# Performance work log

Hardware: AMD Instinct MI355X
Metric: run time of the kernel (lower is better)

The kernel has to match this reference:

```python
import jax, jax.numpy as jnp
import numpy as np
from jax import lax

K = 10
EPS = 1e-12

def _l2norm(v):
    # F.normalize: v / max(||v||_2, eps) along last dim
    n = jnp.sqrt(jnp.sum(v * v, axis=-1, keepdims=True))
    return v / jnp.maximum(n, EPS)

def setup_inputs() -> dict:
    key = jax.random.key(0)
    ks = jax.random.split(key, 10)
    N, F_in, H, C, E = 100000, 512, 128, 40, 1600000
    x = jax.random.normal(ks[0], (N, F_in), dtype=jnp.float32)
    edge_index = jax.random.randint(ks[1], (2, E), 0, N, dtype=jnp.int64)
    s1 = 1.0 / np.sqrt(F_in)
    W1 = jax.random.uniform(ks[2], (F_in, H), jnp.float32, -s1, s1)
    b1 = jax.random.uniform(ks[3], (H,), jnp.float32, -s1, s1)
    s2 = 1.0 / np.sqrt(H)
    proj_w = jax.random.uniform(ks[4], (H, 1), jnp.float32, -s2, s2)
    proj_b = jax.random.uniform(ks[5], (1,), jnp.float32, -s2, s2)
    hop_w = jax.random.normal(ks[6], (1, K + 1), dtype=jnp.float32) * 0.1  # glorot-ish
    W2 = jax.random.uniform(ks[7], (H, C), jnp.float32, -s2, s2)
    b2 = jax.random.uniform(ks[8], (C,), jnp.float32, -s2, s2)
    return {"x": x, "edge_index": edge_index, "W1": W1, "b1": b1,
            "proj_w": proj_w, "proj_b": proj_b, "hop_w": hop_w,
            "W2": W2, "b2": b2}

def reference(x, edge_index, W1, b1, proj_w, proj_b, hop_w, W2, b2):
    N = x.shape[0]
    # Net: dropout (eval -> identity), lin1 + selu
    h = jax.nn.selu(x @ W1 + b1)  # [N, H]

    # --- gcn_norm with added self-loops ---
    loops = jnp.arange(N, dtype=edge_index.dtype)
    row = jnp.concatenate([edge_index[0], loops])
    col = jnp.concatenate([edge_index[1], loops])
    ew = jnp.ones(row.shape[0], dtype=h.dtype)
    deg = jax.ops.segment_sum(ew, col, num_segments=N)  # [N]
    dinv = jnp.where(deg > 0, lax.rsqrt(deg), 0.0)
    norm = dinv[row] * ew * dinv[col]  # [E+N]

    # --- K hops of scatter-add propagation ---
    def hop(xc, _):
        xn = jax.ops.segment_sum(norm[:, None] * xc[row], col, num_segments=N)
        return xn, xn
    _, hops = lax.scan(hop, h, None, length=K)  # [K, N, H]
    pps = jnp.concatenate([h[None], hops], axis=0).transpose(1, 0, 2)  # [N, K+1, H]

    # attention-weighted hop pooling
    feature_pool = (pps @ proj_w + proj_b)[..., 0]      # [N, K+1]
    m = feature_pool.mean(axis=0)                        # [K+1]
    share_w = _l2norm(m + hop_w)                         # [1, K+1]
    self_w = _l2norm(feature_pool)                       # [N, K+1]
    share = jnp.einsum('k,nkh->nh', share_w[0], pps)     # [N, H]
    selfr = jnp.einsum('nk,nkh->nh', self_w, pps)        # [N, H]
    out_prop = 0.2 * share + 0.8 * selfr

    h2 = jnp.tanh(out_prop)
    logits = h2 @ W2 + b2
    return jax.nn.log_softmax(logits, axis=1)
```

## Files before the change

### kernel.cpp

```cpp
#include <hip/hip_runtime.h>

typedef unsigned int uint;
typedef unsigned short ushort;

typedef short short8 __attribute__((ext_vector_type(8)));
typedef float floatx4 __attribute__((ext_vector_type(4)));
typedef uint uintx4 __attribute__((ext_vector_type(4)));

#define FIN 512
#define HF  128
#define NC  40
#define KHOPS 10

__device__ __forceinline__ ushort f2bf(float f) {
    uint u = __float_as_uint(f);
    uint r = (u + 0x7fffu + ((u >> 16) & 1u)) >> 16;
    return (ushort)r;
}
__device__ __forceinline__ float bflo(uint v) { return __uint_as_float(v << 16); }
__device__ __forceinline__ float bfhi(uint v) { return __uint_as_float(v & 0xffff0000u); }
__device__ __forceinline__ uint packbf2(float a, float b) {
    return (uint)f2bf(a) | ((uint)f2bf(b) << 16);
}
__device__ __forceinline__ uint cvtpk(float lo, float hi) {
    uint r;
    asm("v_cvt_pk_bf16_f32 %0, %1, %2" : "=v"(r) : "v"(lo), "v"(hi));
    return r;
}
__device__ __forceinline__ float selu_f(float v) {
    const float l = 1.0507009873554805f, a = 1.6732632423543772f;
    return v > 0.f ? l * v : l * a * (expf(v) - 1.f);
}

#define GLDS16(g, l)                                                        \
    __builtin_amdgcn_global_load_lds(                                       \
        (const __attribute__((address_space(1))) void*)(g),                 \
        (__attribute__((address_space(3))) void*)(l), 16, 0, 0)

__global__ void k_w1frag(const float* __restrict__ W1, ushort* __restrict__ w1f) {
    int id = blockIdx.x * 256 + threadIdx.x;
    if (id >= 16 * 8 * 64) return;
    int l = id & 63;
    int t = (id >> 6) & 7;
    int s = id >> 9;
    int row0 = s * 32 + (l >> 4) * 8;
    int col  = t * 16 + (l & 15);
    ushort* dst = w1f + (size_t)id * 8;
#pragma unroll
    for (int i = 0; i < 8; ++i)
        dst[i] = f2bf(W1[(row0 + i) * HF + col]);
}

__global__ void k_w2frag(const float* __restrict__ W2, ushort* __restrict__ w2f) {
    int id = blockIdx.x * 256 + threadIdx.x;
    if (id >= 12 * 64) return;
    int l = id & 63;
    int tile = id >> 6;
    int kk = tile / 3, t = tile % 3;
    int row0 = kk * 32 + (l >> 4) * 8;
    int col  = t * 16 + (l & 15);
    ushort* dst = w2f + (size_t)id * 8;
#pragma unroll
    for (int i = 0; i < 8; ++i)
        dst[i] = (col < NC) ? f2bf(W2[(row0 + i) * NC + col]) : (ushort)0;
}

__global__ __launch_bounds__(256) void k_gemm(
        const float* __restrict__ x, const ushort* __restrict__ w1f,
        const float* __restrict__ b1, ushort* __restrict__ h,
        const float* __restrict__ projw, const float* __restrict__ projb,
        float* __restrict__ fp0, int N) {
    __shared__ __align__(16) float bufA[4][32 * 32];
    __shared__ __align__(16) float bufB[4][32 * 32];
    int tid = threadIdx.x;
    int lane = tid & 63, w = tid >> 6;
    int rowblk = blockIdx.x * 128 + w * 32;

    int srl = lane >> 3;
    int ssl = lane & 7;
    int srcoff = ((ssl ^ srl) << 2);
    float* bA = bufA[w];
    float* bB = bufB[w];

    floatx4 acc[2][8];
#pragma unroll
    for (int rt = 0; rt < 2; ++rt)
#pragma unroll
        for (int t = 0; t < 8; ++t) acc[rt][t] = (floatx4){0.f, 0.f, 0.f, 0.f};

    short8 bE[8], bO[8];

    auto STAGE = [&](float* lbuf, int kk) {
        int k0 = kk * 32;
#pragma unroll
        for (int i = 0; i < 4; ++i) {
            int row = rowblk + i * 8 + srl;
            const float* g = x + (size_t)min(row, N - 1) * FIN + k0 + srcoff;
            GLDS16(g, lbuf + i * 256);
        }
    };
    auto LOADB = [&](short8* bb, int kk) {
        const ushort* wp = w1f + ((size_t)(kk * 8) * 64 + lane) * 8;
#pragma unroll
        for (int t = 0; t < 8; ++t) bb[t] = *(const short8*)(wp + (size_t)t * 512);
    };

    int rl16 = lane & 15, cq = lane >> 4;
    int lo_sl = ((2 * cq) ^ (rl16 & 7)) << 4;
    int hi_sl = ((2 * cq + 1) ^ (rl16 & 7)) << 4;

    auto COMPUTE = [&](const float* lbuf, short8* bb) {
#pragma unroll
        for (int rt = 0; rt < 2; ++rt) {
            const char* rbase = (const char*)lbuf + (rt * 16 + rl16) * 128;
            float4 lo = *(const float4*)(rbase + lo_sl);
            float4 hi = *(const float4*)(rbase + hi_sl);
            uintx4 pa;
            pa.x = cvtpk(lo.x, lo.y); pa.y = cvtpk(lo.z, lo.w);
            pa.z = cvtpk(hi.x, hi.y); pa.w = cvtpk(hi.z, hi.w);
            short8 af = __builtin_bit_cast(short8, pa);
#pragma unroll
            for (int t = 0; t < 8; ++t)
                acc[rt][t] = __builtin_amdgcn_mfma_f32_16x16x32_bf16(af, bb[t], acc[rt][t], 0, 0, 0);
        }
    };

    STAGE(bA, 0);
    LOADB(bE, 0);
#pragma unroll 1
    for (int kk = 0; kk < 16; kk += 2) {
        asm volatile("s_waitcnt lgkmcnt(0)" ::: "memory");
        __builtin_amdgcn_sched_barrier(0);
        STAGE(bB, kk + 1);
        LOADB(bO, kk + 1);
        asm volatile("s_waitcnt vmcnt(12)" ::: "memory");
        __builtin_amdgcn_sched_barrier(0);
        COMPUTE(bA, bE);
        asm volatile("s_waitcnt lgkmcnt(0)" ::: "memory");
        __builtin_amdgcn_sched_barrier(0);
        if (kk + 2 < 16) {
            STAGE(bA, kk + 2);
            LOADB(bE, kk + 2);
            asm volatile("s_waitcnt vmcnt(12)" ::: "memory");
        } else {
            asm volatile("s_waitcnt vmcnt(0)" ::: "memory");
        }
        __builtin_amdgcn_sched_barrier(0);
        COMPUTE(bB, bO);
    }

    int col0 = lane & 15;
    float fpd[2][4];
#pragma unroll
    for (int rt = 0; rt < 2; ++rt)
#pragma unroll
        for (int q = 0; q < 4; ++q) fpd[rt][q] = 0.f;
#pragma unroll
    for (int t = 0; t < 8; ++t) {
        int col = t * 16 + col0;
        float bias = b1[col];
        float pw = projw[col];
#pragma unroll
        for (int rt = 0; rt < 2; ++rt) {
#pragma unroll
            for (int q = 0; q < 4; ++q) {
                int row = rowblk + rt * 16 + (lane >> 4) * 4 + q;
                float v = selu_f(acc[rt][t][q] + bias);
                if (row < N) h[(size_t)row * HF + col] = f2bf(v);
                fpd[rt][q] = fmaf(v, pw, fpd[rt][q]);
            }
        }
    }
#pragma unroll
    for (int rt = 0; rt < 2; ++rt)
#pragma unroll
        for (int q = 0; q < 4; ++q) {
            float d = fpd[rt][q];
#pragma unroll
            for (int m = 1; m < 16; m <<= 1) d += __shfl_xor(d, m);
            fpd[rt][q] = d;
        }
    if (col0 == 0) {
        float pb = projb[0];
#pragma unroll
        for (int rt = 0; rt < 2; ++rt)
#pragma unroll
            for (int q = 0; q < 4; ++q) {
                int row = rowblk + rt * 16 + (lane >> 4) * 4 + q;
                if (row < N) fp0[row] = fpd[rt][q] + pb;
            }
    }
}

__global__ void k_deg_init(int* __restrict__ deg, int N) {
    int i = blockIdx.x * 256 + threadIdx.x;
    if (i < N) deg[i] = 1;
}
__global__ void k_deg(const int* __restrict__ ei, int* __restrict__ deg, int E) {
    int e = blockIdx.x * 256 + threadIdx.x;
    if (e < E) atomicAdd(&deg[ei[E + e]], 1);
}
__global__ void k_dinv(const int* __restrict__ deg, float* __restrict__ dinv, int N) {
    int i = blockIdx.x * 256 + threadIdx.x;
    if (i < N) dinv[i] = rsqrtf((float)deg[i]);
}

__global__ void k_scan1(const int* __restrict__ deg, int* __restrict__ offs,
                        int* __restrict__ bsum, int N) {
    __shared__ int lds[256];
    int tid = threadIdx.x;
    int base = blockIdx.x * 1024;
    int c[4], s = 0;
#pragma unroll
    for (int i = 0; i < 4; ++i) {
        int g = base + tid * 4 + i;
        c[i] = (g < N) ? (deg[g] - 1) : 0;
        s += c[i];
    }
    lds[tid] = s;
    __syncthreads();
    for (int off = 1; off < 256; off <<= 1) {
        int add = (tid >= off) ? lds[tid - off] : 0;
        __syncthreads();
        lds[tid] += add;
        __syncthreads();
    }
    int run = lds[tid] - s;
#pragma unroll
    for (int i = 0; i < 4; ++i) {
        int g = base + tid * 4 + i;
        if (g < N) offs[g] = run;
        run += c[i];
    }
    if (tid == 0) bsum[blockIdx.x] = lds[255];
}
__global__ void k_scan2(int* __restrict__ bsum, int nb) {
    if (blockIdx.x == 0 && threadIdx.x == 0) {
        int run = 0;
        for (int i = 0; i < nb; ++i) { int v = bsum[i]; bsum[i] = run; run += v; }
    }
}
__global__ void k_scan3(int* __restrict__ offs, const int* __restrict__ bsum, int N, int E) {
    int g = blockIdx.x * 256 + threadIdx.x;
    if (g < N) offs[g] += bsum[g >> 10];
    else if (g == N) offs[N] = E;
}

__global__ void k_fill(const int* __restrict__ ei, const int* __restrict__ offs,
                       int* __restrict__ cursor, int2* __restrict__ edat,
                       const float* __restrict__ dinv, int E) {
    int e = blockIdx.x * 256 + threadIdx.x;
    if (e >= E) return;
    int r = ei[e], c = ei[E + e];
    int p = offs[c] + atomicAdd(&cursor[c], 1);
    edat[p] = make_int2(r, __float_as_int(dinv[r] * dinv[c]));
}

__global__ __launch_bounds__(256) void k_hop(
                      const ushort* __restrict__ xin, ushort* __restrict__ xout,
                      const int* __restrict__ offs, const int2* __restrict__ edat,
                      const float* __restrict__ dinv,
                      const float* __restrict__ projw, const float* __restrict__ projb,
                      float* __restrict__ fpk, int N) {
    int wid = (blockIdx.x * blockDim.x + threadIdx.x) >> 6;
    int lane = threadIdx.x & 63;
    if (wid >= N) return;
    const uint* xin2 = (const uint*)xin;
    float dn = dinv[wid];
    uint sv = xin2[(size_t)wid * 64 + lane];
    float wself = dn * dn;
    float acc0 = wself * bflo(sv);
    float acc1 = wself * bfhi(sv);
    int s = offs[wid], e = offs[wid + 1];
    for (int base = s; base < e; base += 64) {
        int idx = base + lane;
        int idxc = min(idx, e - 1);
        int2 ed = edat[idxc];
        int src = ed.x;
        float ew = (idx < e) ? __int_as_float(ed.y) : 0.f;
        int cnt = min(64, e - base);
        int groups = (cnt + 15) >> 4;
        for (int g = 0; g < groups; ++g) {
            int j = g * 16;
            uint xv[16];
            float wv[16];
#pragma unroll
            for (int u = 0; u < 16; ++u) {
                int sj = __builtin_amdgcn_readlane(src, j + u);
                wv[u] = __int_as_float(__builtin_amdgcn_readlane(__float_as_int(ew), j + u));
                xv[u] = xin2[(size_t)(uint)sj * 64 + lane];
            }
#pragma unroll
            for (int u = 0; u < 16; ++u) {
                acc0 = fmaf(wv[u], bflo(xv[u]), acc0);
                acc1 = fmaf(wv[u], bfhi(xv[u]), acc1);
            }
        }
    }
    ((uint*)xout)[(size_t)wid * 64 + lane] = packbf2(acc0, acc1);
    float dot = acc0 * projw[2 * lane] + acc1 * projw[2 * lane + 1];
#pragma unroll
    for (int m = 1; m < 64; m <<= 1) dot += __shfl_xor(dot, m);
    if (lane == 0) fpk[wid] = dot + projb[0];
}

__global__ void k_msum(const float* __restrict__ fp, float* __restrict__ msum, int N) {
    int k = blockIdx.y;
    int i = blockIdx.x * 256 + threadIdx.x;
    int tid = threadIdx.x;
    float v = (i < N) ? fp[(size_t)k * N + i] : 0.f;
#pragma unroll
    for (int m = 1; m < 64; m <<= 1) v += __shfl_xor(v, m);
    __shared__ float ws4[4];
    if ((tid & 63) == 0) ws4[tid >> 6] = v;
    __syncthreads();
    if (tid == 0) atomicAdd(&msum[k], ws4[0] + ws4[1] + ws4[2] + ws4[3]);
}

__global__ void k_sharew(const float* __restrict__ msum, const float* __restrict__ hopw,
                         float* __restrict__ sharew, int N) {
    int k = threadIdx.x;
    float s = (k < KHOPS + 1) ? (msum[k] / (float)N + hopw[k]) : 0.f;
    float ss = s * s;
#pragma unroll
    for (int m = 1; m < 64; m <<= 1) ss += __shfl_xor(ss, m);
    float inv = 1.f / fmaxf(sqrtf(ss), 1e-12f);
    if (k < KHOPS + 1) sharew[k] = s * inv;
}

__global__ __launch_bounds__(256) void k_out(
                     const ushort* __restrict__ hops, const float* __restrict__ fp,
                     const float* __restrict__ sharew, const ushort* __restrict__ w2f,
                     const float* __restrict__ b2, float* __restrict__ out, int N) {
    __shared__ __align__(16) char As[16 * 256];
    int tid = threadIdx.x;
    int nloc = tid >> 4;
    int fg = tid & 15;
    int node = blockIdx.x * 16 + nloc;
    bool valid = node < N;
    int nodec = valid ? node : N - 1;
    const uint* hops2 = (const uint*)hops;

    float c[KHOPS + 1];
    float ss = 0.f;
#pragma unroll
    for (int k = 0; k <= KHOPS; ++k) {
        float f = fp[(size_t)k * N + nodec];
        c[k] = f;
        ss += f * f;
    }
    float inv = 1.f / fmaxf(sqrtf(ss), 1e-12f);
#pragma unroll
    for (int k = 0; k <= KHOPS; ++k)
        c[k] = valid ? (0.2f * sharew[k] + 0.8f * c[k] * inv) : 0.f;

    const uint* base = hops2 + (size_t)nodec * 64 + fg * 4;
    size_t kstr = (size_t)N * 64;
    float a[8];
#pragma unroll
    for (int j = 0; j < 8; ++j) a[j] = 0.f;
#pragma unroll
    for (int k = 0; k <= KHOPS; ++k) {
        uint4 v = *(const uint4*)(base + (size_t)k * kstr);
        float ck = c[k];
        a[0] = fmaf(ck, bflo(v.x), a[0]);
        a[1] = fmaf(ck, bfhi(v.x), a[1]);
        a[2] = fmaf(ck, bflo(v.y), a[2]);
        a[3] = fmaf(ck, bfhi(v.y), a[3]);
        a[4] = fmaf(ck, bflo(v.z), a[4]);
        a[5] = fmaf(ck, bfhi(v.z), a[5]);
        a[6] = fmaf(ck, bflo(v.w), a[6]);
        a[7] = fmaf(ck, bfhi(v.w), a[7]);
    }
    uint4 pk;
    pk.x = packbf2(tanhf(a[0]), tanhf(a[1]));
    pk.y = packbf2(tanhf(a[2]), tanhf(a[3]));
    pk.z = packbf2(tanhf(a[4]), tanhf(a[5]));
    pk.w = packbf2(tanhf(a[6]), tanhf(a[7]));
    {
        int slotbyte = fg * 16;
        int addr = nloc * 256 + (slotbyte ^ ((nloc & 15) << 4));
        *(uint4*)(As + addr) = pk;
    }
    __syncthreads();

    int w = tid >> 6, lane = tid & 63;
    floatx4 acc = (floatx4){0.f, 0.f, 0.f, 0.f};
    if (w < 3) {
        int r = lane & 15;
#pragma unroll
        for (int kk = 0; kk < 4; ++kk) {
            int slotbyte = kk * 64 + (lane >> 4) * 16;
            int addr = r * 256 + (slotbyte ^ ((r & 15) << 4));
            short8 af = *(const short8*)(As + addr);
            const short8 bf = *(const short8*)(w2f + (size_t)((kk * 3 + w) * 64 + lane) * 8);
            acc = __builtin_amdgcn_mfma_f32_16x16x32_bf16(af, bf, acc, 0, 0, 0);
        }
    }
    __syncthreads();

    float* Ls = (float*)As;
    if (w < 3) {
        int cls = w * 16 + (lane & 15);
        float bb = (cls < NC) ? b2[cls] : 0.f;
#pragma unroll
        for (int q = 0; q < 4; ++q) {
            int row = (lane >> 4) * 4 + q;
            Ls[row * 48 + cls] = acc[q] + bb;
        }
    }
    __syncthreads();

    int r2 = tid >> 4;
    int c16 = tid & 15;
    float v0 = Ls[r2 * 48 + c16];
    float v1 = Ls[r2 * 48 + 16 + c16];
    bool has2 = c16 < 8;
    float v2 = has2 ? Ls[r2 * 48 + 32 + c16] : -INFINITY;
    float lm = fmaxf(fmaxf(v0, v1), v2);
#pragma unroll
    for (int m = 1; m < 16; m <<= 1) lm = fmaxf(lm, __shfl_xor(lm, m));
    float se = expf(v0 - lm) + expf(v1 - lm) + (has2 ? expf(v2 - lm) : 0.f);
#pragma unroll
    for (int m = 1; m < 16; m <<= 1) se += __shfl_xor(se, m);
    float lse = lm + logf(se);
    int nodeo = blockIdx.x * 16 + r2;
    if (nodeo < N) {
        out[(size_t)nodeo * NC + c16] = v0 - lse;
        out[(size_t)nodeo * NC + 16 + c16] = v1 - lse;
        if (has2) out[(size_t)nodeo * NC + 32 + c16] = v2 - lse;
    }
}

extern "C" void kernel_launch(void* const* d_in, const int* in_sizes, int n_in,
                              void* d_out, int out_size, void* d_ws, size_t ws_size,
                              hipStream_t stream) {
    const float* x     = (const float*)d_in[0];
    const int*   ei    = (const int*)d_in[1];
    const float* W1    = (const float*)d_in[2];
    const float* b1    = (const float*)d_in[3];
    const float* projw = (const float*)d_in[4];
    const float* projb = (const float*)d_in[5];
    const float* hopw  = (const float*)d_in[6];
    const float* W2    = (const float*)d_in[7];
    const float* b2    = (const float*)d_in[8];
    float* out = (float*)d_out;

    int N = in_sizes[0] / FIN;
    int E = in_sizes[1] / 2;

    char* p = (char*)d_ws;
    auto alloc = [&](size_t bytes) -> char* {
        char* r = p;
        p += (bytes + 255) & ~(size_t)255;
        return r;
    };
    ushort* hops   = (ushort*)alloc((size_t)(KHOPS + 1) * N * HF * 2);
    int*    deg    = (int*)alloc((size_t)N * 4);
    float*  dinv   = (float*)alloc((size_t)N * 4);
    int*    offs   = (int*)alloc((size_t)(N + 1) * 4);
    int*    cursor = (int*)alloc((size_t)N * 4);
    int*    bsum   = (int*)alloc(4096);
    int2*   edat   = (int2*)alloc((size_t)E * 8);
    float*  fp     = (float*)alloc((size_t)(KHOPS + 1) * N * 4);
    float*  msum   = (float*)alloc(64);
    float*  sharew = (float*)alloc(64);
    ushort* w1f    = (ushort*)alloc((size_t)FIN * HF * 2);
    ushort* w2f    = (ushort*)alloc((size_t)12 * 64 * 8 * 2);

    int nb256N = (N + 255) / 256;
    int nbE    = (E + 255) / 256;
    int nbWave = (N + 3) / 4;
    int nb1024 = (N + 1023) / 1024;

    k_w1frag<<<32, 256, 0, stream>>>(W1, w1f);
    k_w2frag<<<3, 256, 0, stream>>>(W2, w2f);
    k_gemm<<<(N + 127) / 128, 256, 0, stream>>>(x, w1f, b1, hops, projw, projb, fp, N);

    k_deg_init<<<nb256N, 256, 0, stream>>>(deg, N);
    k_deg<<<nbE, 256, 0, stream>>>(ei, deg, E);
    k_dinv<<<nb256N, 256, 0, stream>>>(deg, dinv, N);

    k_scan1<<<nb1024, 256, 0, stream>>>(deg, offs, bsum, N);
    k_scan2<<<1, 64, 0, stream>>>(bsum, nb1024);
    k_scan3<<<(N + 256) / 256, 256, 0, stream>>>(offs, bsum, N, E);

    hipMemsetAsync(cursor, 0, (size_t)N * 4, stream);
    k_fill<<<nbE, 256, 0, stream>>>(ei, offs, cursor, edat, dinv, E);

    for (int k = 1; k <= KHOPS; ++k) {
        const ushort* xin = hops + (size_t)(k - 1) * N * HF;
        ushort* xout      = hops + (size_t)k * N * HF;
        k_hop<<<nbWave, 256, 0, stream>>>(xin, xout, offs, edat, dinv,
                                          projw, projb, fp + (size_t)k * N, N);
    }

    hipMemsetAsync(msum, 0, 64, stream);
    dim3 gm(nb256N, KHOPS + 1);
    k_msum<<<gm, 256, 0, stream>>>(fp, msum, N);
    k_sharew<<<1, 64, 0, stream>>>(msum, hopw, sharew, N);

    k_out<<<(N + 15) / 16, 256, 0, stream>>>(hops, fp, sharew, w2f, b2, out, N);
}
```

Before: 968.3 us.

## Fuse hop loop into one cooperative persistent kernel and fold reductions

Replaces the ten per-hop kernel launches with a single cooperative kernel of 1024 blocks. It loops over hops using grid-wide syncs and accumulates the per-hop feature_pool sums into msum inside the kernel. The separate msum pass is removed, the hop-0 sum is folded into the GEMM epilogue, dinv is folded into the scan, and deg/cursor are zeroed with one memset. The trade-off is that a fixed persistent grid with grid.sync may give lower occupancy or worse load balance than one wave per node with a full launch.

```diff
diff --git a/kernel.cpp b/kernel.cpp
--- a/kernel.cpp
+++ b/kernel.cpp
@@ -1,4 +1,7 @@
 #include <hip/hip_runtime.h>
+#include <hip/hip_cooperative_groups.h>
+
+namespace cg = cooperative_groups;
 
 typedef unsigned int uint;
 typedef unsigned short ushort;
@@ -69,7 +72,7 @@
         const float* __restrict__ x, const ushort* __restrict__ w1f,
         const float* __restrict__ b1, ushort* __restrict__ h,
         const float* __restrict__ projw, const float* __restrict__ projb,
-        float* __restrict__ fp0, int N) {
+        float* __restrict__ fp0, float* __restrict__ msum, int N) {
     __shared__ __align__(16) float bufA[4][32 * 32];
     __shared__ __align__(16) float bufB[4][32 * 32];
     int tid = threadIdx.x;
@@ -180,6 +183,7 @@
             for (int m = 1; m < 16; m <<= 1) d += __shfl_xor(d, m);
             fpd[rt][q] = d;
         }
+    float s0 = 0.f;
     if (col0 == 0) {
         float pb = projb[0];
 #pragma unroll
@@ -187,26 +191,26 @@
 #pragma unroll
             for (int q = 0; q < 4; ++q) {
                 int row = rowblk + rt * 16 + (lane >> 4) * 4 + q;
-                if (row < N) fp0[row] = fpd[rt][q] + pb;
+                if (row < N) {
+                    fp0[row] = fpd[rt][q] + pb;
+                    s0 += fpd[rt][q];
+                }
             }
     }
-}
-
-__global__ void k_deg_init(int* __restrict__ deg, int N) {
-    int i = blockIdx.x * 256 + threadIdx.x;
-    if (i < N) deg[i] = 1;
-}
+    s0 += __shfl_xor(s0, 16);
+    s0 += __shfl_xor(s0, 32);
+    if (lane == 0) bufA[w][0] = s0;
+    __syncthreads();
+    if (tid == 0) atomicAdd(msum, bufA[0][0] + bufA[1][0] + bufA[2][0] + bufA[3][0]);
+}
+
 __global__ void k_deg(const int* __restrict__ ei, int* __restrict__ deg, int E) {
     int e = blockIdx.x * 256 + threadIdx.x;
     if (e < E) atomicAdd(&deg[ei[E + e]], 1);
 }
-__global__ void k_dinv(const int* __restrict__ deg, float* __restrict__ dinv, int N) {
-    int i = blockIdx.x * 256 + threadIdx.x;
-    if (i < N) dinv[i] = rsqrtf((float)deg[i]);
-}
 
 __global__ void k_scan1(const int* __restrict__ deg, int* __restrict__ offs,
-                        int* __restrict__ bsum, int N) {
+                        int* __restrict__ bsum, float* __restrict__ dinv, int N) {
     __shared__ int lds[256];
     int tid = threadIdx.x;
     int base = blockIdx.x * 1024;
@@ -214,8 +218,10 @@
 #pragma unroll
     for (int i = 0; i < 4; ++i) {
         int g = base + tid * 4 + i;
-        c[i] = (g < N) ? (deg[g] - 1) : 0;
-        s += c[i];
+        int dv = (g < N) ? deg[g] : 0;
+        if (g < N) dinv[g] = rsqrtf((float)(dv + 1));
+        c[i] = dv;
+        s += dv;
     }
     lds[tid] = s;
     __syncthreads();
@@ -256,71 +262,82 @@
     edat[p] = make_int2(r, __float_as_int(dinv[r] * dinv[c]));
 }
 
-__global__ __launch_bounds__(256) void k_hop(
-                      const ushort* __restrict__ xin, ushort* __restrict__ xout,
-                      const int* __restrict__ offs, const int2* __restrict__ edat,
-                      const float* __restrict__ dinv,
-                      const float* __restrict__ projw, const float* __restrict__ projb,
-                      float* __restrict__ fpk, int N) {
-    int wid = (blockIdx.x * blockDim.x + threadIdx.x) >> 6;
-    int lane = threadIdx.x & 63;
-    if (wid >= N) return;
-    const uint* xin2 = (const uint*)xin;
-    float dn = dinv[wid];
-    uint sv = xin2[(size_t)wid * 64 + lane];
-    float wself = dn * dn;
-    float acc0 = wself * bflo(sv);
-    float acc1 = wself * bfhi(sv);
-    int s = offs[wid], e = offs[wid + 1];
-    for (int base = s; base < e; base += 64) {
-        int idx = base + lane;
-        int idxc = min(idx, e - 1);
-        int2 ed = edat[idxc];
-        int src = ed.x;
-        float ew = (idx < e) ? __int_as_float(ed.y) : 0.f;
-        int cnt = min(64, e - base);
-        int groups = (cnt + 15) >> 4;
-        for (int g = 0; g < groups; ++g) {
-            int j = g * 16;
-            uint xv[16];
-            float wv[16];
-#pragma unroll
-            for (int u = 0; u < 16; ++u) {
-                int sj = __builtin_amdgcn_readlane(src, j + u);
-                wv[u] = __int_as_float(__builtin_amdgcn_readlane(__float_as_int(ew), j + u));
-                xv[u] = xin2[(size_t)(uint)sj * 64 + lane];
+__global__ __launch_bounds__(256, 4) void k_hops(
+        ushort* __restrict__ hops, const int* __restrict__ offs,
+        const int2* __restrict__ edat, const float* __restrict__ dinv,
+        const float* __restrict__ projw, const float* __restrict__ projb,
+        float* __restrict__ fp, float* __restrict__ msum, int N) {
+    cg::grid_group grid = cg::this_grid();
+    __shared__ float bms[4];
+    int tid = threadIdx.x;
+    int lane = tid & 63, w = tid >> 6;
+    int gwid = blockIdx.x * 4 + w;
+    int nw = gridDim.x * 4;
+    float pw0 = projw[2 * lane], pw1 = projw[2 * lane + 1];
+    float pb = projb[0];
+
+    for (int k = 1; k <= KHOPS; ++k) {
+        const uint* xin2 = (const uint*)(hops + (size_t)(k - 1) * N * HF);
+        uint* xo = (uint*)(hops + (size_t)k * N * HF);
+        float* fpk = fp + (size_t)k * N;
+        float ms = 0.f;
+        for (int wid = gwid; wid < N; wid += nw) {
+            float dn = dinv[wid];
+            uint sv = xin2[(size_t)wid * 64 + lane];
+            float wself = dn * dn;
+            float acc0 = wself * bflo(sv);
+            float acc1 = wself * bfhi(sv);
+            int s = offs[wid], e = offs[wid + 1];
+            for (int base = s; base < e; base += 64) {
+                int idx = base + lane;
+                int idxc = min(idx, e - 1);
+                int2 ed = edat[idxc];
+                int src = ed.x;
+                float ew = (idx < e) ? __int_as_float(ed.y) : 0.f;
+                int cnt = min(64, e - base);
+                int groups = (cnt + 15) >> 4;
+                for (int g = 0; g < groups; ++g) {
+                    int j = g * 16;
+                    uint xv[16];
+                    float wv[16];
+#pragma unroll
+                    for (int u = 0; u < 16; ++u) {
+                        int sj = __builtin_amdgcn_readlane(src, j + u);
+                        wv[u] = __int_as_float(__builtin_amdgcn_readlane(__float_as_int(ew), j + u));
+                        xv[u] = xin2[(size_t)(uint)sj * 64 + lane];
+                    }
+#pragma unroll
+                    for (int u = 0; u < 16; ++u) {
+                        acc0 = fmaf(wv[u], bflo(xv[u]), acc0);
+                        acc1 = fmaf(wv[u], bfhi(xv[u]), acc1);
+                    }
+                }
             }
-#pragma unroll
-            for (int u = 0; u < 16; ++u) {
-                acc0 = fmaf(wv[u], bflo(xv[u]), acc0);
-                acc1 = fmaf(wv[u], bfhi(xv[u]), acc1);
-            }
-        }
-    }
-    ((uint*)xout)[(size_t)wid * 64 + lane] = packbf2(acc0, acc1);
-    float dot = acc0 * projw[2 * lane] + acc1 * projw[2 * lane + 1];
-#pragma unroll
-    for (int m = 1; m < 64; m <<= 1) dot += __shfl_xor(dot, m);
-    if (lane == 0) fpk[wid] = dot + projb[0];
-}
-
-__global__ void k_msum(const float* __restrict__ fp, float* __restrict__ msum, int N) {
-    int k = blockIdx.y;
-    int i = blockIdx.x * 256 + threadIdx.x;
-    int tid = threadIdx.x;
-    float v = (i < N) ? fp[(size_t)k * N + i] : 0.f;
-#pragma unroll
-    for (int m = 1; m < 64; m <<= 1) v += __shfl_xor(v, m);
-    __shared__ float ws4[4];
-    if ((tid & 63) == 0) ws4[tid >> 6] = v;
-    __syncthreads();
-    if (tid == 0) atomicAdd(&msum[k], ws4[0] + ws4[1] + ws4[2] + ws4[3]);
+            xo[(size_t)wid * 64 + lane] = packbf2(acc0, acc1);
+            float dot = acc0 * pw0 + acc1 * pw1;
+#pragma unroll
+            for (int m = 1; m < 64; m <<= 1) dot += __shfl_xor(dot, m);
+            dot += pb;
+            if (lane == 0) { fpk[wid] = dot; ms += dot; }
+        }
+        if (lane == 0) bms[w] = ms;
+        __syncthreads();
+        if (tid == 0) atomicAdd(&msum[k], bms[0] + bms[1] + bms[2] + bms[3]);
+        if (k < KHOPS) {
+            __threadfence();
+            grid.sync();
+        }
+    }
 }
 
 __global__ void k_sharew(const float* __restrict__ msum, const float* __restrict__ hopw,
-                         float* __restrict__ sharew, int N) {
+                         float* __restrict__ sharew, const float* __restrict__ projb, int N) {
     int k = threadIdx.x;
-    float s = (k < KHOPS + 1) ? (msum[k] / (float)N + hopw[k]) : 0.f;
+    float s = 0.f;
+    if (k < KHOPS + 1) {
+        s = msum[k] / (float)N + hopw[k];
+        if (k == 0) s += projb[0];
+    }
     float ss = s * s;
 #pragma unroll
     for (int m = 1; m < 64; m <<= 1) ss += __shfl_xor(ss, m);
@@ -457,9 +474,9 @@
     };
     ushort* hops   = (ushort*)alloc((size_t)(KHOPS + 1) * N * HF * 2);
     int*    deg    = (int*)alloc((size_t)N * 4);
+    int*    cursor = (int*)alloc((size_t)N * 4);
     float*  dinv   = (float*)alloc((size_t)N * 4);
     int*    offs   = (int*)alloc((size_t)(N + 1) * 4);
-    int*    cursor = (int*)alloc((size_t)N * 4);
     int*    bsum   = (int*)alloc(4096);
     int2*   edat   = (int2*)alloc((size_t)E * 8);
     float*  fp     = (float*)alloc((size_t)(KHOPS + 1) * N * 4);
@@ -468,37 +485,29 @@
     ushort* w1f    = (ushort*)alloc((size_t)FIN * HF * 2);
     ushort* w2f    = (ushort*)alloc((size_t)12 * 64 * 8 * 2);
 
-    int nb256N = (N + 255) / 256;
     int nbE    = (E + 255) / 256;
-    int nbWave = (N + 3) / 4;
     int nb1024 = (N + 1023) / 1024;
+
+    size_t zlen = (size_t)((char*)cursor - (char*)deg) + (size_t)N * 4;
+    hipMemsetAsync(deg, 0, zlen, stream);
+    hipMemsetAsync(msum, 0, 64, stream);
 
     k_w1frag<<<32, 256, 0, stream>>>(W1, w1f);
     k_w2frag<<<3, 256, 0, stream>>>(W2, w2f);
-    k_gemm<<<(N + 127) / 128, 256, 0, stream>>>(x, w1f, b1, hops, projw, projb, fp, N);
-
-    k_deg_init<<<nb256N, 256, 0, stream>>>(deg, N);
+    k_gemm<<<(N + 127) / 128, 256, 0, stream>>>(x, w1f, b1, hops, projw, projb, fp, msum, N);
+
     k_deg<<<nbE, 256, 0, stream>>>(ei, deg, E);
-    k_dinv<<<nb256N, 256, 0, stream>>>(deg, dinv, N);
-
-    k_scan1<<<nb1024, 256, 0, stream>>>(deg, offs, bsum, N);
+    k_scan1<<<nb1024, 256, 0, stream>>>(deg, offs, bsum, dinv, N);
     k_scan2<<<1, 64, 0, stream>>>(bsum, nb1024);
     k_scan3<<<(N + 256) / 256, 256, 0, stream>>>(offs, bsum, N, E);
-
-    hipMemsetAsync(cursor, 0, (size_t)N * 4, stream);
     k_fill<<<nbE, 256, 0, stream>>>(ei, offs, cursor, edat, dinv, E);
 
-    for (int k = 1; k <= KHOPS; ++k) {
-        const ushort* xin = hops + (size_t)(k - 1) * N * HF;
-        ushort* xout      = hops + (size_t)k * N * HF;
-        k_hop<<<nbWave, 256, 0, stream>>>(xin, xout, offs, edat, dinv,
-                                          projw, projb, fp + (size_t)k * N, N);
-    }
-
-    hipMemsetAsync(msum, 0, 64, stream);
-    dim3 gm(nb256N, KHOPS + 1);
-    k_msum<<<gm, 256, 0, stream>>>(fp, msum, N);
-    k_sharew<<<1, 64, 0, stream>>>(msum, hopw, sharew, N);
-
+    {
+        void* args[] = {(void*)&hops, (void*)&offs, (void*)&edat, (void*)&dinv,
+                        (void*)&projw, (void*)&projb, (void*)&fp, (void*)&msum, (void*)&N};
+        hipLaunchCooperativeKernel((void*)k_hops, dim3(1024), dim3(256), args, 0, stream);
+    }
+
+    k_sharew<<<1, 64, 0, stream>>>(msum, hopw, sharew, projb, N);
     k_out<<<(N + 15) / 16, 256, 0, stream>>>(hops, fp, sharew, w2f, b2, out, N);
 }
```

Result: slower. 2.902 ms (+199.7%).
